# Optimization experiments

Measured on AMD Instinct MI355X. Metric: run time of the kernel, lower is better.

Reference implementation:

```python
import jax, jax.numpy as jnp
import numpy as np

B, S, D, H = 4, 2048, 256, 4
DH = D // H  # per-head dim (shared for q, k, v)


def setup_inputs() -> dict:
    key = jax.random.key(0)
    ks = jax.random.split(key, 10)
    scale = 1.0 / np.sqrt(D)
    return {
        "q": jax.random.normal(ks[0], (B, S, D), jnp.float32),
        "k": jax.random.normal(ks[1], (B, S, D), jnp.float32),
        "v": jax.random.normal(ks[2], (B, S, D), jnp.float32),
        "mask": jax.random.randint(ks[3], (B, S, S), 0, 2).astype(bool),
        # per-head query/key projections: [H, D, DH] (+ bias [H, DH])
        "Wq": jax.random.uniform(ks[4], (H, D, DH), jnp.float32, -scale, scale),
        "bq": jax.random.uniform(ks[5], (H, DH), jnp.float32, -scale, scale),
        "Wk": jax.random.uniform(ks[6], (H, D, DH), jnp.float32, -scale, scale),
        "bk": jax.random.uniform(ks[7], (H, DH), jnp.float32, -scale, scale),
        # shared value projection: [D, DH]
        "Wv": jax.random.uniform(ks[8], (D, DH), jnp.float32, -scale, scale),
        "bv": jnp.zeros((DH,), jnp.float32),
        # final projection (no bias): [DH, D]
        "Wf": jax.random.uniform(ks[9], (DH, D), jnp.float32, -scale, scale),
    }


def reference(q, k, v, mask, Wq, bq, Wk, bk, Wv, bv, Wf):
    # per-head projections (all heads at once): [B, H, S, DH]
    q_h = jnp.einsum("bsd,hde->bhse", q, Wq) + bq[None, :, None, :]
    k_h = jnp.einsum("bsd,hde->bhse", k, Wk) + bk[None, :, None, :]
    # shared value projection: [B, S, DH]
    v_p = v @ Wv + bv
    # scaled scores: [B, H, S, S]
    scores = jnp.einsum("bhse,bhte->bhst", q_h, k_h) / jnp.sqrt(
        jnp.asarray(DH, q_h.dtype)
    )
    scores = jnp.where(mask[:, None, :, :], jnp.asarray(-1e9, scores.dtype), scores)
    attn = jax.nn.softmax(scores, axis=-1)  # [B, H, S, S]
    # shared V for every head: [B, H, S, DH]
    heads = jnp.einsum("bhst,bte->bhse", attn, v_p)
    mean_head = heads.mean(axis=1)  # [B, S, DH]
    out = mean_head @ Wf  # [B, S, D]
    return out, attn
```

## Files before the change

### kernel.cpp

```cpp
#include <hip/hip_runtime.h>
#include <stdint.h>
#include <stddef.h>

#define B_ 4
#define S_ 2048
#define D_ 256
#define H_ 4
#define DH_ 64
#define NTT 64
#define SC_LOG2E 0.18033688011112042f

typedef __attribute__((ext_vector_type(8))) short short8;
typedef __attribute__((ext_vector_type(4))) short short4v;
typedef __attribute__((ext_vector_type(4))) float f32x4;
typedef unsigned int uint;

__device__ __forceinline__ short bf16_rne(float f) {
  union { float f; uint32_t u; } c; c.f = f;
  uint32_t u = c.u + 0x7FFFu + ((c.u >> 16) & 1u);
  return (short)(u >> 16);
}

__device__ __forceinline__ f32x4 mfma16(short8 a, short8 b, f32x4 c) {
  return __builtin_amdgcn_mfma_f32_16x16x32_bf16(a, b, c, 0, 0, 0);
}

__device__ __forceinline__ void gl_lds16(const short* g, short* l) {
  __builtin_amdgcn_global_load_lds(
      (const __attribute__((address_space(1))) unsigned int*)g,
      (__attribute__((address_space(3))) unsigned int*)l, 16, 0, 0);
}

__global__ void detect_kernel(const unsigned int* __restrict__ m, int* __restrict__ flag) {
  __shared__ int isbool;
  if (threadIdx.x == 0) isbool = 0;
  __syncthreads();
#pragma unroll
  for (int i = 0; i < 4; ++i) {
    unsigned int d = m[threadIdx.x + i * 256];
    if (d & 0xFFFFFFFEu) isbool = 1;
  }
  __syncthreads();
  if (threadIdx.x == 0) *flag = isbool ? 0 : 1;
}

__global__ __launch_bounds__(256) void prep_pack(
    const unsigned char* __restrict__ maskB, const int* __restrict__ flagp,
    uint* __restrict__ mbits,
    const float* __restrict__ Wq, const float* __restrict__ Wk, const float* __restrict__ Wv,
    short* __restrict__ WqT, short* __restrict__ WkT, short* __restrict__ WvT) {
  const int bx = blockIdx.x;
  if (bx < 2048) {
    int tid = bx * 256 + threadIdx.x;
    uint w = 0;
    if (*flagp) {
      const uint4* p = (const uint4*)((const uint*)maskB + (size_t)tid * 32);
#pragma unroll
      for (int i = 0; i < 8; ++i) {
        uint4 d = p[i];
        w |= (d.x ? 1u : 0u) << (i * 4);
        w |= (d.y ? 1u : 0u) << (i * 4 + 1);
        w |= (d.z ? 1u : 0u) << (i * 4 + 2);
        w |= (d.w ? 1u : 0u) << (i * 4 + 3);
      }
    } else {
      const uint4* p = (const uint4*)(maskB + (size_t)tid * 32);
#pragma unroll
      for (int i = 0; i < 2; ++i) {
        uint4 d = p[i];
        const uint* dw = (const uint*)&d;
#pragma unroll
        for (int j = 0; j < 4; ++j) {
          uint x = dw[j];
          int base = i * 16 + j * 4;
          w |= ((x & 0x000000FFu) ? 1u : 0u) << (base);
          w |= ((x & 0x0000FF00u) ? 1u : 0u) << (base + 1);
          w |= ((x & 0x00FF0000u) ? 1u : 0u) << (base + 2);
          w |= ((x & 0xFF000000u) ? 1u : 0u) << (base + 3);
        }
      }
    }
    mbits[tid] = w;
  } else {
    int tid = (bx - 2048) * 256 + threadIdx.x;
    if (tid < 65536) {
      int n = tid >> 8, d = tid & 255;
      int hh = n >> 6, e = n & 63;
      WqT[tid] = bf16_rne(Wq[((size_t)hh * D_ + d) * DH_ + e] * SC_LOG2E);
      WkT[tid] = bf16_rne(Wk[((size_t)hh * D_ + d) * DH_ + e]);
    } else {
      int t2 = tid - 65536;
      int e = t2 >> 8, d = t2 & 255;
      WvT[t2] = bf16_rne(Wv[(size_t)d * DH_ + e]);
    }
  }
}

__global__ __launch_bounds__(256) void proj_all(
    const float* __restrict__ q, const float* __restrict__ k, const float* __restrict__ v,
    const short* __restrict__ WqT, const short* __restrict__ WkT, const short* __restrict__ WvT,
    const float* __restrict__ bq, const float* __restrict__ bk, const float* __restrict__ bv,
    short* __restrict__ qh, short* __restrict__ kh, short* __restrict__ vT) {
  const int yy = blockIdx.y;
  const float* X; const short* WT; const float* bias; short* outp;
  int vmode, n0; float bscale;
  if (yy < 4)      { X = q; WT = WqT; bias = bq; outp = qh; vmode = 0; bscale = SC_LOG2E; n0 = yy * 64; }
  else if (yy < 8) { X = k; WT = WkT; bias = bk; outp = kh; vmode = 0; bscale = 1.0f; n0 = (yy - 4) * 64; }
  else             { X = v; WT = WvT; bias = bv; outp = vT; vmode = 1; bscale = 1.0f; n0 = 0; }

  const int b = blockIdx.z;
  const int s0 = blockIdx.x * 64;
  const int tid = threadIdx.x;
  const int wave = tid >> 6, lane = tid & 63;
  const int lr = lane & 15, lg = lane >> 4;

  const int arowi = s0 + wave * 16 + lr;
  const float* xr = X + ((size_t)b * S_ + arowi) * D_;

  f32x4 zero4 = {0.f, 0.f, 0.f, 0.f};
  f32x4 acc[4];
#pragma unroll
  for (int ct = 0; ct < 4; ++ct) acc[ct] = zero4;

#pragma unroll
  for (int c = 0; c < 8; ++c) {
    const int k0 = c * 32 + lg * 8;
    f32x4 x0 = *(const f32x4*)(xr + k0);
    f32x4 x1 = *(const f32x4*)(xr + k0 + 4);
    short8 a;
#pragma unroll
    for (int jj = 0; jj < 4; ++jj) { a[jj] = bf16_rne(x0[jj]); a[4 + jj] = bf16_rne(x1[jj]); }
#pragma unroll
    for (int ct = 0; ct < 4; ++ct) {
      short8 bw = *(const short8*)(WT + (size_t)(n0 + ct * 16 + lr) * D_ + k0);
      acc[ct] = mfma16(a, bw, acc[ct]);
    }
  }

  if (vmode == 0) {
#pragma unroll
    for (int ct = 0; ct < 4; ++ct) {
      int n = n0 + ct * 16 + lr;
      float bb = bias[n] * bscale;
      int hh = n >> 6, e = n & 63;
#pragma unroll
      for (int r = 0; r < 4; ++r) {
        int srow = s0 + wave * 16 + lg * 4 + r;
        outp[(((size_t)b * H_ + hh) * S_ + srow) * DH_ + e] = bf16_rne(acc[ct][r] + bb);
      }
    }
  } else {
#pragma unroll
    for (int ct = 0; ct < 4; ++ct) {
      int n = n0 + ct * 16 + lr;
      float bb = bias[n];
      int s4 = s0 + wave * 16 + lg * 4;
      short4v pk;
#pragma unroll
      for (int r = 0; r < 4; ++r) pk[r] = bf16_rne(acc[ct][r] + bb);
      *(short4v*)(outp + ((size_t)b * DH_ + n) * S_ + s4) = pk;
    }
  }
}

__device__ __forceinline__ void stageK64(const short* Ksrc, short* dst, int wq, int lane) {
#pragma unroll
  for (int i = 0; i < 2; ++i) {
    int ub = i * 256 + wq * 64;
    int u = ub + lane;
    int row = u >> 3, c = (u ^ row) & 7;
    gl_lds16(Ksrc + (size_t)row * 64 + c * 8, dst + (size_t)ub * 8);
  }
}

__device__ __forceinline__ void stageV64(const short* Vb, int t0, short* dst, int wq, int lane) {
#pragma unroll
  for (int i = 0; i < 2; ++i) {
    int ub = i * 256 + wq * 64;
    int u = ub + lane;
    int er = u >> 3, c = (u ^ er) & 7;
    gl_lds16(Vb + (size_t)er * S_ + t0 + c * 8, dst + (size_t)ub * 8);
  }
}

__global__ __launch_bounds__(512, 4) void attn_kernel(
    const short* __restrict__ qh, const short* __restrict__ kh,
    const short* __restrict__ vT, const uint* __restrict__ mbits,
    float* __restrict__ attn, float* __restrict__ heads) {
  __shared__ __align__(16) short Kt[2][2][4096];
  __shared__ __align__(16) short Vt[2][2][4096];
  __shared__ __align__(16) short Pt[8][1024];

  const int flat = blockIdx.x;
  const int xcd = flat & 7;
  const int pos = flat >> 3;
  const int bh_i = xcd * 2 + (pos >> 5);
  const int q0 = (pos & 31) * 64;
  const int b = bh_i >> 2, h = bh_i & 3;

  const int tid = threadIdx.x;
  const int wave = tid >> 6, lane = tid & 63;
  const int half = wave >> 2, wq = wave & 3;
  const int lr = lane & 15, lg = lane >> 4;
  const int tbase = half * (S_ / 2);

  const size_t bh = (size_t)b * H_ + h;
  const short* Qb = qh + bh * S_ * DH_;
  const short* Kb = kh + bh * S_ * DH_;
  const short* Vb = vT + (size_t)b * DH_ * S_;

  const int qrow = q0 + wq * 16 + lr;
  const uint* mrow = mbits + ((size_t)b * S_ + qrow) * (S_ / 32);
  float* arow = attn + (bh * S_ + qrow) * S_;

  const short8 aq0 = *(const short8*)(Qb + (size_t)qrow * DH_ + lg * 8);
  const short8 aq1 = *(const short8*)(Qb + (size_t)qrow * DH_ + 32 + lg * 8);

  short* pw = &Pt[wave][0];

  float rsum = 0.f;
  stageK64(Kb + (size_t)tbase * DH_, Kt[half][0], wq, lane);
  asm volatile("s_waitcnt vmcnt(0)" ::: "memory");
  __builtin_amdgcn_s_barrier();
  int cur = 0;
  for (int tt = 0; tt < 16; ++tt) {
    const int t0 = tbase + tt * NTT;
    uint2 mv = *(const uint2*)(mrow + (t0 >> 5));
    if (tt + 1 < 16) {
      stageK64(Kb + (size_t)(t0 + NTT) * DH_, Kt[half][cur ^ 1], wq, lane);
      asm volatile("s_waitcnt vmcnt(3)" ::: "memory");
    } else {
      asm volatile("s_waitcnt vmcnt(1)" ::: "memory");
    }
    __builtin_amdgcn_s_barrier();
    __builtin_amdgcn_s_setprio(1);
    const short* kt = Kt[half][cur];
#pragma unroll
    for (int j = 0; j < 4; ++j) {
      int row = j * 16 + lr;
      short8 bk0 = *(const short8*)(kt + row * 64 + (((lg) ^ row) & 7) * 8);
      short8 bk1 = *(const short8*)(kt + row * 64 + (((lg + 4) ^ row) & 7) * 8);
      f32x4 acc = {0.f, 0.f, 0.f, 0.f};
      acc = mfma16(bk0, aq0, acc);
      acc = mfma16(bk1, aq1, acc);
      uint mw = (j < 2) ? mv.x : mv.y;
#pragma unroll
      for (int r = 0; r < 4; ++r) {
        int sh = (j & 1) * 16 + lg * 4 + r;
        float p = ((mw >> sh) & 1u) ? 0.f : __builtin_exp2f(acc[r]);
        rsum += p;
      }
    }
    __builtin_amdgcn_s_setprio(0);
    __builtin_amdgcn_s_barrier();
    cur ^= 1;
  }
  rsum += __shfl_xor(rsum, 16);
  rsum += __shfl_xor(rsum, 32);
  float* fsum = (float*)&Pt[0][0];
  if (lane < 16) fsum[wave * 16 + lr] = rsum;
  __syncthreads();
  const float rinv = 1.0f / (fsum[wq * 16 + lr] + fsum[(wq + 4) * 16 + lr]);

  f32x4 o[4];
#pragma unroll
  for (int ct = 0; ct < 4; ++ct) o[ct] = (f32x4){0.f, 0.f, 0.f, 0.f};

  stageK64(Kb + (size_t)tbase * DH_, Kt[half][0], wq, lane);
  stageV64(Vb, tbase, Vt[half][0], wq, lane);
  asm volatile("s_waitcnt vmcnt(0)" ::: "memory");
  __syncthreads();
  cur = 0;
  for (int tt = 0; tt < 16; ++tt) {
    const int t0 = tbase + tt * NTT;
    uint2 mv = *(const uint2*)(mrow + (t0 >> 5));
    if (tt + 1 < 16) {
      stageK64(Kb + (size_t)(t0 + NTT) * DH_, Kt[half][cur ^ 1], wq, lane);
      stageV64(Vb, t0 + NTT, Vt[half][cur ^ 1], wq, lane);
      asm volatile("s_waitcnt vmcnt(9)" ::: "memory");
    } else {
      asm volatile("s_waitcnt vmcnt(5)" ::: "memory");
    }
    __builtin_amdgcn_s_barrier();
    __builtin_amdgcn_s_setprio(1);
    const short* kt = Kt[half][cur];
    const short* vt = Vt[half][cur];
#pragma unroll
    for (int j = 0; j < 4; ++j) {
      int row = j * 16 + lr;
      short8 bk0 = *(const short8*)(kt + row * 64 + (((lg) ^ row) & 7) * 8);
      short8 bk1 = *(const short8*)(kt + row * 64 + (((lg + 4) ^ row) & 7) * 8);
      f32x4 acc = {0.f, 0.f, 0.f, 0.f};
      acc = mfma16(bk0, aq0, acc);
      acc = mfma16(bk1, aq1, acc);
      uint mw = (j < 2) ? mv.x : mv.y;
      f32x4 pst;
      short4v pk;
#pragma unroll
      for (int r = 0; r < 4; ++r) {
        int sh = (j & 1) * 16 + lg * 4 + r;
        float p = ((mw >> sh) & 1u) ? 0.f : __builtin_exp2f(acc[r]) * rinv;
        pst[r] = p;
        pk[r] = bf16_rne(p);
      }
      *(f32x4*)(arow + t0 + j * 16 + lg * 4) = pst;
      *(short4v*)(pw + lr * 64 + (((2 * j + (lg >> 1)) ^ lr) & 7) * 8 + (lg & 1) * 4) = pk;
    }
    short8 apf[2];
#pragma unroll
    for (int kc = 0; kc < 2; ++kc)
      apf[kc] = *(const short8*)(pw + lr * 64 + (((4 * kc + lg) ^ lr) & 7) * 8);
#pragma unroll
    for (int ct = 0; ct < 4; ++ct) {
      int er = ct * 16 + lr;
#pragma unroll
      for (int kc = 0; kc < 2; ++kc) {
        short8 bvf = *(const short8*)(vt + er * 64 + (((4 * kc + lg) ^ er) & 7) * 8);
        o[ct] = mfma16(bvf, apf[kc], o[ct]);
      }
    }
    __builtin_amdgcn_s_setprio(0);
    __builtin_amdgcn_s_barrier();
    cur ^= 1;
  }

  float* ocomb = (float*)&Pt[0][0];
  if (half == 1) {
#pragma unroll
    for (int ct = 0; ct < 4; ++ct)
      *(f32x4*)(ocomb + wq * 1024 + lr * 64 + ct * 16 + lg * 4) = o[ct];
  }
  __syncthreads();
  if (half == 0) {
#pragma unroll
    for (int ct = 0; ct < 4; ++ct) {
      f32x4 t = *(const f32x4*)(ocomb + wq * 1024 + lr * 64 + ct * 16 + lg * 4);
      f32x4 s = o[ct];
      s[0] += t[0]; s[1] += t[1]; s[2] += t[2]; s[3] += t[3];
      *(f32x4*)(heads + (bh * S_ + qrow) * DH_ + ct * 16 + lg * 4) = s;
    }
  }
}

__global__ __launch_bounds__(256) void final_kernel(
    const float* __restrict__ heads, const float* __restrict__ Wf,
    float* __restrict__ outp) {
  __shared__ float mean[16][DH_];
  const int row0 = blockIdx.x * 16;
  const int tid = threadIdx.x;
#pragma unroll
  for (int i = 0; i < 4; ++i) {
    int idx = tid + i * 256;
    int r = idx >> 6, e = idx & 63;
    int gs = row0 + r;
    int bb = gs >> 11, ss = gs & (S_ - 1);
    float acc = 0.f;
#pragma unroll
    for (int hh = 0; hh < H_; ++hh)
      acc += heads[(((size_t)bb * H_ + hh) * S_ + ss) * DH_ + e];
    mean[r][e] = acc * 0.25f;
  }
  __syncthreads();
  float acc[16];
#pragma unroll
  for (int r = 0; r < 16; ++r) acc[r] = 0.f;
  for (int e = 0; e < DH_; ++e) {
    float wf = Wf[(size_t)e * D_ + tid];
#pragma unroll
    for (int r = 0; r < 16; ++r) acc[r] += mean[r][e] * wf;
  }
#pragma unroll
  for (int r = 0; r < 16; ++r)
    outp[(size_t)(row0 + r) * D_ + tid] = acc[r];
}

extern "C" void kernel_launch(void* const* d_in, const int* in_sizes, int n_in,
                              void* d_out, int out_size, void* d_ws, size_t ws_size,
                              hipStream_t stream) {
  (void)in_sizes; (void)n_in; (void)out_size; (void)ws_size;
  const float* q  = (const float*)d_in[0];
  const float* k  = (const float*)d_in[1];
  const float* v  = (const float*)d_in[2];
  const unsigned char* mask = (const unsigned char*)d_in[3];
  const float* Wq = (const float*)d_in[4];
  const float* bq = (const float*)d_in[5];
  const float* Wk = (const float*)d_in[6];
  const float* bk = (const float*)d_in[7];
  const float* Wv = (const float*)d_in[8];
  const float* bv = (const float*)d_in[9];
  const float* Wf = (const float*)d_in[10];

  float* out  = (float*)d_out;
  float* attn = out + (size_t)B_ * S_ * D_;

  char* ws = (char*)d_ws;
  short* qh    = (short*)(ws);
  short* kh    = (short*)(ws + 4194304);
  short* vT    = (short*)(ws + 8388608);
  short* WqT   = (short*)(ws + 9437184);
  short* WkT   = (short*)(ws + 9568256);
  short* WvT   = (short*)(ws + 9699328);
  float* heads = (float*)(ws + 9732096);
  int*   flag  = (int*)(ws + 18120704);
  uint*  mbits = (uint*)(ws + 18120768);

  detect_kernel<<<1, 256, 0, stream>>>((const unsigned int*)mask, flag);
  prep_pack<<<2368, 256, 0, stream>>>(mask, flag, mbits, Wq, Wk, Wv, WqT, WkT, WvT);
  proj_all<<<dim3(32, 9, B_), 256, 0, stream>>>(q, k, v, WqT, WkT, WvT, bq, bk, bv, qh, kh, vT);
  attn_kernel<<<512, 512, 0, stream>>>(qh, kh, vT, mbits, attn, heads);
  final_kernel<<<512, 256, 0, stream>>>(heads, Wf, out);
}
```

Before: 166.5 us.

## Split softmax row-sum pass into a separate lighter kernel

The first attention pass, which computes masked exp row sums, moves out of the fused attention kernel into its own rsum_kernel. That kernel uses less LDS (no V or P tiles) and declares a higher occupancy bound. The reciprocal sums go to a workspace buffer that the attention kernel reads back. This adds a kernel launch, a global write and read of the row sums, and a second read of Q, K and the mask. In exchange, the sum pass can run at higher occupancy.

```diff
diff --git a/kernel.cpp b/kernel.cpp
--- a/kernel.cpp
+++ b/kernel.cpp
@@ -183,13 +183,11 @@
   }
 }
 
-__global__ __launch_bounds__(512, 4) void attn_kernel(
+__global__ __launch_bounds__(512, 6) void rsum_kernel(
     const short* __restrict__ qh, const short* __restrict__ kh,
-    const short* __restrict__ vT, const uint* __restrict__ mbits,
-    float* __restrict__ attn, float* __restrict__ heads) {
+    const uint* __restrict__ mbits, float* __restrict__ rinvg) {
   __shared__ __align__(16) short Kt[2][2][4096];
-  __shared__ __align__(16) short Vt[2][2][4096];
-  __shared__ __align__(16) short Pt[8][1024];
+  __shared__ float fs[8][16];
 
   const int flat = blockIdx.x;
   const int xcd = flat & 7;
@@ -207,16 +205,12 @@
   const size_t bh = (size_t)b * H_ + h;
   const short* Qb = qh + bh * S_ * DH_;
   const short* Kb = kh + bh * S_ * DH_;
-  const short* Vb = vT + (size_t)b * DH_ * S_;
 
   const int qrow = q0 + wq * 16 + lr;
   const uint* mrow = mbits + ((size_t)b * S_ + qrow) * (S_ / 32);
-  float* arow = attn + (bh * S_ + qrow) * S_;
 
   const short8 aq0 = *(const short8*)(Qb + (size_t)qrow * DH_ + lg * 8);
   const short8 aq1 = *(const short8*)(Qb + (size_t)qrow * DH_ + 32 + lg * 8);
-
-  short* pw = &Pt[wave][0];
 
   float rsum = 0.f;
   stageK64(Kb + (size_t)tbase * DH_, Kt[half][0], wq, lane);
@@ -257,10 +251,48 @@
   }
   rsum += __shfl_xor(rsum, 16);
   rsum += __shfl_xor(rsum, 32);
-  float* fsum = (float*)&Pt[0][0];
-  if (lane < 16) fsum[wave * 16 + lr] = rsum;
-  __syncthreads();
-  const float rinv = 1.0f / (fsum[wq * 16 + lr] + fsum[(wq + 4) * 16 + lr]);
+  if (lane < 16) fs[wave][lr] = rsum;
+  __syncthreads();
+  if (half == 0 && lane < 16)
+    rinvg[bh * S_ + q0 + wq * 16 + lane] = 1.0f / (fs[wq][lane] + fs[wq + 4][lane]);
+}
+
+__global__ __launch_bounds__(512, 4) void attn_kernel(
+    const short* __restrict__ qh, const short* __restrict__ kh,
+    const short* __restrict__ vT, const uint* __restrict__ mbits,
+    const float* __restrict__ rinvg,
+    float* __restrict__ attn, float* __restrict__ heads) {
+  __shared__ __align__(16) short Kt[2][2][4096];
+  __shared__ __align__(16) short Vt[2][2][4096];
+  __shared__ __align__(16) short Pt[8][1024];
+
+  const int flat = blockIdx.x;
+  const int xcd = flat & 7;
+  const int pos = flat >> 3;
+  const int bh_i = xcd * 2 + (pos >> 5);
+  const int q0 = (pos & 31) * 64;
+  const int b = bh_i >> 2, h = bh_i & 3;
+
+  const int tid = threadIdx.x;
+  const int wave = tid >> 6, lane = tid & 63;
+  const int half = wave >> 2, wq = wave & 3;
+  const int lr = lane & 15, lg = lane >> 4;
+  const int tbase = half * (S_ / 2);
+
+  const size_t bh = (size_t)b * H_ + h;
+  const short* Qb = qh + bh * S_ * DH_;
+  const short* Kb = kh + bh * S_ * DH_;
+  const short* Vb = vT + (size_t)b * DH_ * S_;
+
+  const int qrow = q0 + wq * 16 + lr;
+  const uint* mrow = mbits + ((size_t)b * S_ + qrow) * (S_ / 32);
+  float* arow = attn + (bh * S_ + qrow) * S_;
+
+  const short8 aq0 = *(const short8*)(Qb + (size_t)qrow * DH_ + lg * 8);
+  const short8 aq1 = *(const short8*)(Qb + (size_t)qrow * DH_ + 32 + lg * 8);
+  const float rinv = rinvg[bh * S_ + qrow];
+
+  short* pw = &Pt[wave][0];
 
   f32x4 o[4];
 #pragma unroll
@@ -270,7 +302,7 @@
   stageV64(Vb, tbase, Vt[half][0], wq, lane);
   asm volatile("s_waitcnt vmcnt(0)" ::: "memory");
   __syncthreads();
-  cur = 0;
+  int cur = 0;
   for (int tt = 0; tt < 16; ++tt) {
     const int t0 = tbase + tt * NTT;
     uint2 mv = *(const uint2*)(mrow + (t0 >> 5));
@@ -403,10 +435,12 @@
   float* heads = (float*)(ws + 9732096);
   int*   flag  = (int*)(ws + 18120704);
   uint*  mbits = (uint*)(ws + 18120768);
+  float* rinvg = (float*)(ws + 20217920);
 
   detect_kernel<<<1, 256, 0, stream>>>((const unsigned int*)mask, flag);
   prep_pack<<<2368, 256, 0, stream>>>(mask, flag, mbits, Wq, Wk, Wv, WqT, WkT, WvT);
   proj_all<<<dim3(32, 9, B_), 256, 0, stream>>>(q, k, v, WqT, WkT, WvT, bq, bk, bv, qh, kh, vT);
-  attn_kernel<<<512, 512, 0, stream>>>(qh, kh, vT, mbits, attn, heads);
+  rsum_kernel<<<512, 512, 0, stream>>>(qh, kh, mbits, rinvg);
+  attn_kernel<<<512, 512, 0, stream>>>(qh, kh, vT, mbits, rinvg, attn, heads);
   final_kernel<<<512, 256, 0, stream>>>(heads, Wf, out);
 }
```

After: 176.4 us. +5.9%, slower.
